# Performance work log

Measured on AMD Instinct MI355X. Metric: run time of the kernel, lower is better.

The kernel has to match this reference:

```python
import jax, jax.numpy as jnp
import numpy as np
from jax import lax

VOCAB = 27
N_EMBD = 512
D_MODEL = 256
PAD_IDX = 26
OUT = 1
B, T = 256, 512


def _lstm_layer(x, w_ih, w_hh, b_ih, b_hh):
    # x: [B, T, in]; w_ih: [4H, in]; w_hh: [4H, H]
    Bb = x.shape[0]
    H = w_hh.shape[1]
    # precompute input contribution to all gates for all timesteps
    xg = jnp.einsum('bti,gi->btg', x, w_ih) + b_ih + b_hh  # [B, T, 4H]

    def step(carry, xg_t):
        h, c = carry
        g = xg_t + h @ w_hh.T  # [B, 4H]
        i, f, gg, o = jnp.split(g, 4, axis=-1)  # PyTorch gate order i,f,g,o
        i = jax.nn.sigmoid(i)
        f = jax.nn.sigmoid(f)
        gg = jnp.tanh(gg)
        o = jax.nn.sigmoid(o)
        c = f * c + i * gg
        h = o * jnp.tanh(c)
        return (h, c), h

    h0 = jnp.zeros((Bb, H), dtype=x.dtype)
    c0 = jnp.zeros((Bb, H), dtype=x.dtype)
    _, ys = lax.scan(step, (h0, c0), jnp.swapaxes(xg, 0, 1))
    return jnp.swapaxes(ys, 0, 1)  # [B, T, H]


def setup_inputs() -> dict:
    key = jax.random.key(0)
    ks = jax.random.split(key, 16)
    s_e = 1.0  # nn.Embedding default init is N(0,1)
    emb = jax.random.normal(ks[0], (VOCAB, N_EMBD), dtype=jnp.float32)
    emb = emb.at[PAD_IDX].set(0.0)
    bound = 1.0 / np.sqrt(D_MODEL)

    def u(k, shape, b):
        return jax.random.uniform(k, shape, dtype=jnp.float32, minval=-b, maxval=b)

    inp = {
        'input_ids': jax.random.randint(ks[1], (B, T), 0, VOCAB, dtype=jnp.int64)
                      if jax.config.jax_enable_x64 else
                      jax.random.randint(ks[1], (B, T), 0, VOCAB).astype(jnp.int32),
        'emb': emb,
        'w_ih0': u(ks[2], (4 * D_MODEL, N_EMBD), bound),
        'w_hh0': u(ks[3], (4 * D_MODEL, D_MODEL), bound),
        'b_ih0': u(ks[4], (4 * D_MODEL,), bound),
        'b_hh0': u(ks[5], (4 * D_MODEL,), bound),
        'w_ih1': u(ks[6], (4 * D_MODEL, D_MODEL), bound),
        'w_hh1': u(ks[7], (4 * D_MODEL, D_MODEL), bound),
        'b_ih1': u(ks[8], (4 * D_MODEL,), bound),
        'b_hh1': u(ks[9], (4 * D_MODEL,), bound),
        'fc1_w': u(ks[10], (D_MODEL // 2, D_MODEL), bound),
        'fc1_b': u(ks[11], (D_MODEL // 2,), bound),
        'fc2_w': u(ks[12], (OUT, D_MODEL // 2), 1.0 / np.sqrt(D_MODEL // 2)),
        'fc2_b': u(ks[13], (OUT,), 1.0 / np.sqrt(D_MODEL // 2)),
    }
    return inp


def reference(input_ids, emb, w_ih0, w_hh0, b_ih0, b_hh0,
              w_ih1, w_hh1, b_ih1, b_hh1, fc1_w, fc1_b, fc2_w, fc2_b):
    # embedding with padding_idx: pad row forced to zero
    table = emb.at[PAD_IDX].set(0.0)
    x = table[input_ids]  # [B, T, n_embd]
    h1 = _lstm_layer(x, w_ih0, w_hh0, b_ih0, b_hh0)   # [B, T, H]
    h2 = _lstm_layer(h1, w_ih1, w_hh1, b_ih1, b_hh1)  # [B, T, H]
    last = h2[:, -1, :]                                # [B, H]
    hidden = jax.nn.relu(last @ fc1_w.T + fc1_b)
    logits = hidden @ fc2_w.T + fc2_b                  # [B, 1]
    return logits
```

## Files before the change

### kernel.cpp

```cpp
#include <hip/hip_runtime.h>

typedef unsigned short u16;
typedef unsigned int u32;
typedef unsigned long long u64;
typedef float f32x2 __attribute__((ext_vector_type(2)));

#define BATCH 256
#define TT 512
#define HID 256
#define GATES 1024
#define NEMB 512
#define VOC 27
#define HPAD 260

__device__ __forceinline__ float bf1(u16 x){ union{u32 u; float f;} v; v.u = ((u32)x) << 16; return v.f; }
__device__ __forceinline__ u16 f2bf(float f){
  union{float f; u32 u;} v; v.f = f;
  u32 u = v.u;
  return (u16)((u + 0x7fffu + ((u >> 16) & 1u)) >> 16);
}
__device__ __forceinline__ float sigm(float x){ return 1.f / (1.f + __expf(-x)); }
__device__ __forceinline__ f32x2 lo2(float4 v){ f32x2 r; r.x = v.x; r.y = v.y; return r; }
__device__ __forceinline__ f32x2 hi2(float4 v){ f32x2 r; r.x = v.z; r.y = v.w; return r; }

__global__ void k_detect(const u16* __restrict__ b, int* __restrict__ flag) {
  int bad = 0;
  for (int k = threadIdx.x; k < 512; k += 64)
    if (((b[2 * k] >> 7) & 0xFF) >= 127) bad = 1;
  unsigned long long m = __ballot(bad);
  if (threadIdx.x == 0) flag[0] = (m != 0ULL) ? 0 : 1;
}

__global__ void k_convert(const void* __restrict__ src, float* __restrict__ dst,
                          int n, const int* __restrict__ flag) {
  int i = blockIdx.x * 256 + threadIdx.x;
  if (i >= n) return;
  dst[i] = flag[0] ? bf1(((const u16*)src)[i]) : ((const float*)src)[i];
}

__global__ void k_prep(const void* __restrict__ emb, const void* __restrict__ wih,
                       const void* __restrict__ bih, const void* __restrict__ bhh,
                       const int* __restrict__ flag, float* __restrict__ W0) {
  int idx = blockIdx.x * 256 + threadIdx.x;
  if (idx >= VOC * GATES) return;
  int v = idx >> 10, g = idx & (GATES - 1);
  int isbf = flag[0];
  float acc = isbf ? (bf1(((const u16*)bih)[g]) + bf1(((const u16*)bhh)[g]))
                   : (((const float*)bih)[g] + ((const float*)bhh)[g]);
  if (v != 26) {
    float s = 0.f;
    if (isbf) {
      const u16* e = (const u16*)emb + v * NEMB;
      const u16* w = (const u16*)wih + g * NEMB;
      for (int i = 0; i < NEMB; i++) s = fmaf(bf1(e[i]), bf1(w[i]), s);
    } else {
      const float* e = (const float*)emb + v * NEMB;
      const float* w = (const float*)wih + g * NEMB;
      for (int i = 0; i < NEMB; i++) s = fmaf(e[i], w[i], s);
    }
    acc += s;
  }
  W0[idx] = acc;
}

__global__ __launch_bounds__(1024) void k_lstm(
    const int* __restrict__ ids, const float* __restrict__ W0,
    const float* __restrict__ whh0, const float* __restrict__ wih1,
    const float* __restrict__ whh1,
    const float* __restrict__ bih1, const float* __restrict__ bhh1,
    float* __restrict__ h0a, float* __restrict__ h0b,
    float* __restrict__ h1a, float* __restrict__ h1b,
    u32* __restrict__ bar)
{
  const int tid = threadIdx.x;
  const int bid = blockIdx.x;
  const int grp = ((bid >> 3) << 1) | (bid & 1);
  const int jq  = (bid & 7) >> 1;
  const int wv  = tid >> 6;
  const int ln  = tid & 63;

  const int tb = tid & 3;
  const int rr = tid >> 2;
  const int grow = (rr >> 6) * 256 + jq * 64 + (rr & 63);

  __shared__ __align__(16) float hp0[2][4][HPAD];
  __shared__ __align__(16) float hp1[4][HPAD];
  __shared__ float gs0[256][5];
  __shared__ float gs1[256][5];
  __shared__ int   ids_l[4][TT];

  const float* wl0 = whh0 + (size_t)grow * HID;
  const float* wi  = wih1 + (size_t)grow * HID;
  const float* wh  = whh1 + (size_t)grow * HID;
  const float bsum = bih1[grow] + bhh1[grow];

  const int pb = tid & 3, pj = (tid >> 2) & 63;
  const int prow = (grp * 4 + pb) * HID + (jq * 64 + pj);
  float c0r = 0.f, c1r = 0.f;

  u32* flags0 = bar;
  u32* flags1 = bar + 4096;

  #pragma unroll
  for (int u = 0; u < 2; ++u) {
    int e = tid + 1024 * u;
    int b = e >> 9, tt = e & 511;
    ids_l[b][tt] = ids[(grp * 4 + b) * TT + tt];
  }

  for (int t = 0; t <= TT + 1; ++t) {
    if (wv == 0) {
      const int q = ln & 3;
      const int pbid = ((bid >> 3) << 3) | (q << 1) | (bid & 1);
      u32 need = 0;
      const u32* fp = nullptr;
      if (ln < 4) {
        if (q != jq && t >= 1 && t <= TT) { fp = flags0 + pbid * 16; need = (u32)t; }
      } else if (ln < 8) {
        if (q != jq && t >= 3) { fp = flags1 + pbid * 16; need = (u32)(t - 2); }
      }
      for (;;) {
        bool ok = true;
        if (need) ok = __hip_atomic_load(fp, __ATOMIC_RELAXED, __HIP_MEMORY_SCOPE_AGENT) >= need;
        if (__all(ok)) break;
        __builtin_amdgcn_s_sleep(2);
      }
    }
    __syncthreads();

    if (tid < 512) {
      if (t <= TT) {
        const float* h0p = ((t + 1) & 1) ? h0b : h0a;
        const u64* s0 = (const u64*)h0p;
        int e = tid;
        u64 v = __hip_atomic_load(s0 + grp * 512 + e, __ATOMIC_RELAXED, __HIP_MEMORY_SCOPE_AGENT);
        *(u64*)&hp0[t & 1][e >> 7][(e & 127) * 2] = v;
      }
    } else {
      if (t >= 2) {
        const float* h1p = ((t + 1) & 1) ? h1b : h1a;
        const u64* s1 = (const u64*)h1p;
        int e = tid - 512;
        u64 v = __hip_atomic_load(s1 + grp * 512 + e, __ATOMIC_RELAXED, __HIP_MEMORY_SCOPE_AGENT);
        *(u64*)&hp1[e >> 7][(e & 127) * 2] = v;
      }
    }
    __syncthreads();

    if (t < TT) {
      float xgv = W0[(size_t)ids_l[tb][t] * GATES + grow];
      const float4* w4 = (const float4*)wl0;
      const float4* h4 = (const float4*)hp0[t & 1][tb];
      f32x2 sA = {0.f, 0.f}, sB = {0.f, 0.f};
      #pragma unroll 8
      for (int k = 0; k < 64; ++k) {
        float4 q = w4[k], hv = h4[k];
        sA = lo2(q) * lo2(hv) + sA;
        sB = hi2(q) * hi2(hv) + sB;
      }
      gs0[rr][tb] = xgv + sA.x + sA.y + sB.x + sB.y;
    }
    __syncthreads();

    if (t < TT && tid < 256) {
      float gi = sigm(gs0[pj][pb]);
      float gf = sigm(gs0[64 + pj][pb]);
      float gg = tanhf(gs0[128 + pj][pb]);
      float go = sigm(gs0[192 + pj][pb]);
      c0r = fmaf(gf, c0r, gi * gg);
      float* h0n = (t & 1) ? h0b : h0a;
      __hip_atomic_store(&h0n[prow], go * tanhf(c0r),
                         __ATOMIC_RELAXED, __HIP_MEMORY_SCOPE_AGENT);
    }
    __syncthreads();
    if (tid == 0 && t < TT)
      __hip_atomic_store(flags0 + bid * 16, (u32)(t + 1),
                         __ATOMIC_RELAXED, __HIP_MEMORY_SCOPE_AGENT);

    if (t >= 2) {
      const float4* wi4 = (const float4*)wi;
      const float4* wh4 = (const float4*)wh;
      const float4* x4  = (const float4*)hp0[(t - 1) & 1][tb];
      const float4* h4  = (const float4*)hp1[tb];
      f32x2 sIa = {0.f,0.f}, sIb = {0.f,0.f}, sHa = {0.f,0.f}, sHb = {0.f,0.f};
      #pragma unroll 8
      for (int k = 0; k < 64; ++k) {
        float4 qi = wi4[k], qh = wh4[k], xv = x4[k], hv = h4[k];
        sIa = lo2(qi) * lo2(xv) + sIa;
        sIb = hi2(qi) * hi2(xv) + sIb;
        sHa = lo2(qh) * lo2(hv) + sHa;
        sHb = hi2(qh) * hi2(hv) + sHb;
      }
      gs1[rr][tb] = bsum + sIa.x + sIa.y + sIb.x + sIb.y
                         + sHa.x + sHa.y + sHb.x + sHb.y;
    }
    __syncthreads();

    if (t >= 2 && tid < 256) {
      float gi = sigm(gs1[pj][pb]);
      float gf = sigm(gs1[64 + pj][pb]);
      float gg = tanhf(gs1[128 + pj][pb]);
      float go = sigm(gs1[192 + pj][pb]);
      c1r = fmaf(gf, c1r, gi * gg);
      float* h1n = (t & 1) ? h1b : h1a;
      __hip_atomic_store(&h1n[prow], go * tanhf(c1r),
                         __ATOMIC_RELAXED, __HIP_MEMORY_SCOPE_AGENT);
    }
    __syncthreads();
    if (tid == 0 && t >= 2 && t <= TT)
      __hip_atomic_store(flags1 + bid * 16, (u32)(t - 1),
                         __ATOMIC_RELAXED, __HIP_MEMORY_SCOPE_AGENT);
  }
}

__global__ __launch_bounds__(128) void k_fc(
    const float* __restrict__ hfin,
    const void* __restrict__ fc1w, const void* __restrict__ fc1b,
    const void* __restrict__ fc2w, const void* __restrict__ fc2b,
    const int* __restrict__ flag, void* __restrict__ out) {
  int b = blockIdx.x, j = threadIdx.x;
  __shared__ float red[128];
  const float* h = hfin + b * HID;
  int isbf = flag[0];
  float acc = isbf ? bf1(((const u16*)fc1b)[j]) : ((const float*)fc1b)[j];
  if (isbf) {
    const u16* w = (const u16*)fc1w + j * HID;
    for (int k = 0; k < HID; k++) acc = fmaf(bf1(w[k]), h[k], acc);
  } else {
    const float* w = (const float*)fc1w + j * HID;
    for (int k = 0; k < HID; k++) acc = fmaf(w[k], h[k], acc);
  }
  acc = fmaxf(acc, 0.f);
  float w2 = isbf ? bf1(((const u16*)fc2w)[j]) : ((const float*)fc2w)[j];
  red[j] = acc * w2;
  __syncthreads();
  for (int s = 64; s > 0; s >>= 1) {
    if (j < s) red[j] += red[j + s];
    __syncthreads();
  }
  if (j == 0) {
    float b2 = isbf ? bf1(((const u16*)fc2b)[0]) : ((const float*)fc2b)[0];
    float r = red[0] + b2;
    if (isbf) ((u16*)out)[b] = f2bf(r);
    else      ((float*)out)[b] = r;
  }
}

extern "C" void kernel_launch(void* const* d_in, const int* in_sizes, int n_in,
                              void* d_out, int out_size, void* d_ws, size_t ws_size,
                              hipStream_t stream) {
  const int* ids   = (const int*)d_in[0];
  const void* emb  = d_in[1];
  const void* wih0 = d_in[2];
  const void* whh0 = d_in[3];
  const void* bih0 = d_in[4];
  const void* bhh0 = d_in[5];
  const void* wih1 = d_in[6];
  const void* whh1 = d_in[7];
  const void* bih1 = d_in[8];
  const void* bhh1 = d_in[9];
  const void* fc1w = d_in[10];
  const void* fc1b = d_in[11];
  const void* fc2w = d_in[12];
  const void* fc2b = d_in[13];

  float* ws = (float*)d_ws;
  int*   flag    = (int*)ws;
  float* W0emb   = ws + 16;
  float* whh0_f  = W0emb  + VOC * GATES;
  float* wih1_f  = whh0_f + GATES * HID;
  float* whh1_f  = wih1_f + GATES * HID;
  float* bih1_f  = whh1_f + GATES * HID;
  float* bhh1_f  = bih1_f + GATES;
  float* h0A = bhh1_f + GATES;
  float* h0B = h0A + BATCH * HID;
  float* c0  = h0B + BATCH * HID;
  float* h1A = c0  + BATCH * HID;
  float* h1B = h1A + BATCH * HID;
  float* c1  = h1B + BATCH * HID;
  u32*   bar = (u32*)c0;

  k_detect<<<1, 64, 0, stream>>>((const u16*)bih0, flag);

  k_convert<<<(GATES * HID + 255) / 256, 256, 0, stream>>>(whh0, whh0_f, GATES * HID, flag);
  k_convert<<<(GATES * HID + 255) / 256, 256, 0, stream>>>(wih1, wih1_f, GATES * HID, flag);
  k_convert<<<(GATES * HID + 255) / 256, 256, 0, stream>>>(whh1, whh1_f, GATES * HID, flag);
  k_convert<<<(GATES + 255) / 256, 256, 0, stream>>>(bih1, bih1_f, GATES, flag);
  k_convert<<<(GATES + 255) / 256, 256, 0, stream>>>(bhh1, bhh1_f, GATES, flag);

  hipMemsetAsync(h0A, 0, (size_t)6 * BATCH * HID * sizeof(float), stream);

  k_prep<<<(VOC * GATES + 255) / 256, 256, 0, stream>>>(emb, wih0, bih0, bhh0, flag, W0emb);

  k_lstm<<<256, 1024, 0, stream>>>(ids, W0emb, whh0_f, wih1_f, whh1_f,
                                   bih1_f, bhh1_f, h0A, h0B, h1A, h1B, bar);

  k_fc<<<BATCH, 128, 0, stream>>>(h1B, fc1w, fc1b, fc2w, fc2b, flag, d_out);
}
```

Before: 12.44 ms.

## Split K across lanes with shuffle reduce and fuse gate nonlinearity per thread

Each thread now computes partial dot products for all four gates of one hidden unit over a quarter of K, then reduces across lanes with xor shuffles. The thread holding ks==0 applies the LSTM cell update directly. This removes the gs0/gs1 shared-memory staging and two __syncthreads per timestep, and the h buffers are padded per K-slice to avoid bank conflicts. The cost is four weight streams per thread, higher register pressure, and only a quarter of the threads doing the activation math.

```diff
diff --git a/kernel.cpp b/kernel.cpp
--- a/kernel.cpp
+++ b/kernel.cpp
@@ -11,7 +11,8 @@
 #define GATES 1024
 #define NEMB 512
 #define VOC 27
-#define HPAD 260
+#define KSF 68
+#define HROW 276
 
 __device__ __forceinline__ float bf1(u16 x){ union{u32 u; float f;} v; v.u = ((u32)x) << 16; return v.f; }
 __device__ __forceinline__ u16 f2bf(float f){
@@ -80,22 +81,35 @@
   const int ln  = tid & 63;
 
   const int tb = tid & 3;
-  const int rr = tid >> 2;
-  const int grow = (rr >> 6) * 256 + jq * 64 + (rr & 63);
-
-  __shared__ __align__(16) float hp0[2][4][HPAD];
-  __shared__ __align__(16) float hp1[4][HPAD];
-  __shared__ float gs0[256][5];
-  __shared__ float gs1[256][5];
+  const int ks = (tid >> 2) & 3;
+  const int j  = tid >> 4;
+
+  __shared__ __align__(16) float hp0[2][4][HROW];
+  __shared__ __align__(16) float hp1[4][HROW];
   __shared__ int   ids_l[4][TT];
 
-  const float* wl0 = whh0 + (size_t)grow * HID;
-  const float* wi  = wih1 + (size_t)grow * HID;
-  const float* wh  = whh1 + (size_t)grow * HID;
-  const float bsum = bih1[grow] + bhh1[grow];
-
-  const int pb = tid & 3, pj = (tid >> 2) & 63;
-  const int prow = (grp * 4 + pb) * HID + (jq * 64 + pj);
+  const int jj = jq * 64 + j;
+  const size_t r0 = (size_t)jj * HID + ks * 64;
+  const size_t rstep = (size_t)256 * HID;
+  const float4* wl0_0 = (const float4*)(whh0 + r0);
+  const float4* wl0_1 = (const float4*)(whh0 + r0 + rstep);
+  const float4* wl0_2 = (const float4*)(whh0 + r0 + 2 * rstep);
+  const float4* wl0_3 = (const float4*)(whh0 + r0 + 3 * rstep);
+  const float4* wi_0 = (const float4*)(wih1 + r0);
+  const float4* wi_1 = (const float4*)(wih1 + r0 + rstep);
+  const float4* wi_2 = (const float4*)(wih1 + r0 + 2 * rstep);
+  const float4* wi_3 = (const float4*)(wih1 + r0 + 3 * rstep);
+  const float4* wh_0 = (const float4*)(whh1 + r0);
+  const float4* wh_1 = (const float4*)(whh1 + r0 + rstep);
+  const float4* wh_2 = (const float4*)(whh1 + r0 + 2 * rstep);
+  const float4* wh_3 = (const float4*)(whh1 + r0 + 3 * rstep);
+
+  float bs[4];
+  #pragma unroll
+  for (int g = 0; g < 4; ++g) bs[g] = bih1[g * 256 + jj] + bhh1[g * 256 + jj];
+
+  const int prow = (grp * 4 + tb) * HID + jj;
+  const bool owner = (ks == 0);
   float c0r = 0.f, c1r = 0.f;
 
   u32* flags0 = bar;
@@ -133,44 +147,56 @@
         const float* h0p = ((t + 1) & 1) ? h0b : h0a;
         const u64* s0 = (const u64*)h0p;
         int e = tid;
+        int sb = e >> 7, f = (e & 127) * 2;
+        int mf = f + ((f >> 6) << 2);
         u64 v = __hip_atomic_load(s0 + grp * 512 + e, __ATOMIC_RELAXED, __HIP_MEMORY_SCOPE_AGENT);
-        *(u64*)&hp0[t & 1][e >> 7][(e & 127) * 2] = v;
+        *(u64*)&hp0[t & 1][sb][mf] = v;
       }
     } else {
       if (t >= 2) {
         const float* h1p = ((t + 1) & 1) ? h1b : h1a;
         const u64* s1 = (const u64*)h1p;
         int e = tid - 512;
+        int sb = e >> 7, f = (e & 127) * 2;
+        int mf = f + ((f >> 6) << 2);
         u64 v = __hip_atomic_load(s1 + grp * 512 + e, __ATOMIC_RELAXED, __HIP_MEMORY_SCOPE_AGENT);
-        *(u64*)&hp1[e >> 7][(e & 127) * 2] = v;
+        *(u64*)&hp1[sb][mf] = v;
       }
     }
     __syncthreads();
 
     if (t < TT) {
-      float xgv = W0[(size_t)ids_l[tb][t] * GATES + grow];
-      const float4* w4 = (const float4*)wl0;
-      const float4* h4 = (const float4*)hp0[t & 1][tb];
-      f32x2 sA = {0.f, 0.f}, sB = {0.f, 0.f};
-      #pragma unroll 8
-      for (int k = 0; k < 64; ++k) {
-        float4 q = w4[k], hv = h4[k];
-        sA = lo2(q) * lo2(hv) + sA;
-        sB = hi2(q) * hi2(hv) + sB;
-      }
-      gs0[rr][tb] = xgv + sA.x + sA.y + sB.x + sB.y;
-    }
-    __syncthreads();
-
-    if (t < TT && tid < 256) {
-      float gi = sigm(gs0[pj][pb]);
-      float gf = sigm(gs0[64 + pj][pb]);
-      float gg = tanhf(gs0[128 + pj][pb]);
-      float go = sigm(gs0[192 + pj][pb]);
-      c0r = fmaf(gf, c0r, gi * gg);
-      float* h0n = (t & 1) ? h0b : h0a;
-      __hip_atomic_store(&h0n[prow], go * tanhf(c0r),
-                         __ATOMIC_RELAXED, __HIP_MEMORY_SCOPE_AGENT);
+      const float4* h4 = (const float4*)&hp0[t & 1][tb][ks * KSF];
+      f32x2 aL0={0,0}, aH0={0,0}, aL1={0,0}, aH1={0,0};
+      f32x2 aL2={0,0}, aH2={0,0}, aL3={0,0}, aH3={0,0};
+      #pragma unroll 4
+      for (int k = 0; k < 16; ++k) {
+        float4 hv = h4[k];
+        float4 q0 = wl0_0[k], q1 = wl0_1[k], q2 = wl0_2[k], q3 = wl0_3[k];
+        aL0 = lo2(q0) * lo2(hv) + aL0; aH0 = hi2(q0) * hi2(hv) + aH0;
+        aL1 = lo2(q1) * lo2(hv) + aL1; aH1 = hi2(q1) * hi2(hv) + aH1;
+        aL2 = lo2(q2) * lo2(hv) + aL2; aH2 = hi2(q2) * hi2(hv) + aH2;
+        aL3 = lo2(q3) * lo2(hv) + aL3; aH3 = hi2(q3) * hi2(hv) + aH3;
+      }
+      float s0 = aL0.x + aL0.y + aH0.x + aH0.y;
+      float s1 = aL1.x + aL1.y + aH1.x + aH1.y;
+      float s2 = aL2.x + aL2.y + aH2.x + aH2.y;
+      float s3 = aL3.x + aL3.y + aH3.x + aH3.y;
+      s0 += __shfl_xor(s0, 4); s0 += __shfl_xor(s0, 8);
+      s1 += __shfl_xor(s1, 4); s1 += __shfl_xor(s1, 8);
+      s2 += __shfl_xor(s2, 4); s2 += __shfl_xor(s2, 8);
+      s3 += __shfl_xor(s3, 4); s3 += __shfl_xor(s3, 8);
+      if (owner) {
+        const float* xr = W0 + (size_t)ids_l[tb][t] * GATES + jj;
+        float gi = sigm(s0 + xr[0]);
+        float gf = sigm(s1 + xr[256]);
+        float gg = tanhf(s2 + xr[512]);
+        float go = sigm(s3 + xr[768]);
+        c0r = fmaf(gf, c0r, gi * gg);
+        float* h0n = (t & 1) ? h0b : h0a;
+        __hip_atomic_store(&h0n[prow], go * tanhf(c0r),
+                           __ATOMIC_RELAXED, __HIP_MEMORY_SCOPE_AGENT);
+      }
     }
     __syncthreads();
     if (tid == 0 && t < TT)
@@ -178,33 +204,42 @@
                          __ATOMIC_RELAXED, __HIP_MEMORY_SCOPE_AGENT);
 
     if (t >= 2) {
-      const float4* wi4 = (const float4*)wi;
-      const float4* wh4 = (const float4*)wh;
-      const float4* x4  = (const float4*)hp0[(t - 1) & 1][tb];
-      const float4* h4  = (const float4*)hp1[tb];
-      f32x2 sIa = {0.f,0.f}, sIb = {0.f,0.f}, sHa = {0.f,0.f}, sHb = {0.f,0.f};
-      #pragma unroll 8
-      for (int k = 0; k < 64; ++k) {
-        float4 qi = wi4[k], qh = wh4[k], xv = x4[k], hv = h4[k];
-        sIa = lo2(qi) * lo2(xv) + sIa;
-        sIb = hi2(qi) * hi2(xv) + sIb;
-        sHa = lo2(qh) * lo2(hv) + sHa;
-        sHb = hi2(qh) * hi2(hv) + sHb;
-      }
-      gs1[rr][tb] = bsum + sIa.x + sIa.y + sIb.x + sIb.y
-                         + sHa.x + sHa.y + sHb.x + sHb.y;
-    }
-    __syncthreads();
-
-    if (t >= 2 && tid < 256) {
-      float gi = sigm(gs1[pj][pb]);
-      float gf = sigm(gs1[64 + pj][pb]);
-      float gg = tanhf(gs1[128 + pj][pb]);
-      float go = sigm(gs1[192 + pj][pb]);
-      c1r = fmaf(gf, c1r, gi * gg);
-      float* h1n = (t & 1) ? h1b : h1a;
-      __hip_atomic_store(&h1n[prow], go * tanhf(c1r),
-                         __ATOMIC_RELAXED, __HIP_MEMORY_SCOPE_AGENT);
+      const float4* x4 = (const float4*)&hp0[(t - 1) & 1][tb][ks * KSF];
+      const float4* h4 = (const float4*)&hp1[tb][ks * KSF];
+      f32x2 aL0={0,0}, aH0={0,0}, aL1={0,0}, aH1={0,0};
+      f32x2 aL2={0,0}, aH2={0,0}, aL3={0,0}, aH3={0,0};
+      #pragma unroll 2
+      for (int k = 0; k < 16; ++k) {
+        float4 xv = x4[k], hv = h4[k];
+        float4 qi0 = wi_0[k], qi1 = wi_1[k], qi2 = wi_2[k], qi3 = wi_3[k];
+        aL0 = lo2(qi0) * lo2(xv) + aL0; aH0 = hi2(qi0) * hi2(xv) + aH0;
+        aL1 = lo2(qi1) * lo2(xv) + aL1; aH1 = hi2(qi1) * hi2(xv) + aH1;
+        aL2 = lo2(qi2) * lo2(xv) + aL2; aH2 = hi2(qi2) * hi2(xv) + aH2;
+        aL3 = lo2(qi3) * lo2(xv) + aL3; aH3 = hi2(qi3) * hi2(xv) + aH3;
+        float4 qh0 = wh_0[k], qh1 = wh_1[k], qh2 = wh_2[k], qh3 = wh_3[k];
+        aL0 = lo2(qh0) * lo2(hv) + aL0; aH0 = hi2(qh0) * hi2(hv) + aH0;
+        aL1 = lo2(qh1) * lo2(hv) + aL1; aH1 = hi2(qh1) * hi2(hv) + aH1;
+        aL2 = lo2(qh2) * lo2(hv) + aL2; aH2 = hi2(qh2) * hi2(hv) + aH2;
+        aL3 = lo2(qh3) * lo2(hv) + aL3; aH3 = hi2(qh3) * hi2(hv) + aH3;
+      }
+      float s0 = aL0.x + aL0.y + aH0.x + aH0.y;
+      float s1 = aL1.x + aL1.y + aH1.x + aH1.y;
+      float s2 = aL2.x + aL2.y + aH2.x + aH2.y;
+      float s3 = aL3.x + aL3.y + aH3.x + aH3.y;
+      s0 += __shfl_xor(s0, 4); s0 += __shfl_xor(s0, 8);
+      s1 += __shfl_xor(s1, 4); s1 += __shfl_xor(s1, 8);
+      s2 += __shfl_xor(s2, 4); s2 += __shfl_xor(s2, 8);
+      s3 += __shfl_xor(s3, 4); s3 += __shfl_xor(s3, 8);
+      if (owner) {
+        float gi = sigm(s0 + bs[0]);
+        float gf = sigm(s1 + bs[1]);
+        float gg = tanhf(s2 + bs[2]);
+        float go = sigm(s3 + bs[3]);
+        c1r = fmaf(gf, c1r, gi * gg);
+        float* h1n = (t & 1) ? h1b : h1a;
+        __hip_atomic_store(&h1n[prow], go * tanhf(c1r),
+                           __ATOMIC_RELAXED, __HIP_MEMORY_SCOPE_AGENT);
+      }
     }
     __syncthreads();
     if (tid == 0 && t >= 2 && t <= TT)
```

Result: slower. 18.59 ms (+49.4%).

## Split block into concurrent layer-0 and layer-1 halves, two gate rows per thread

Applied to the files above, without the earlier changes.

Threads 0-511 now compute the layer-0 recurrent gate matvec while threads 512-1023 compute the layer-1 gate matvec in the same phase, each thread handling two gate rows that share one h vector load. This removes a separate compute phase and one __syncthreads per timestep, and reuses each LDS h load across two weight rows. In exchange the per-thread work doubles and the two halves are unbalanced (layer 1 does twice the FLOPs), so the critical path per step may lengthen and register pressure rises.

```diff
diff --git a/kernel.cpp b/kernel.cpp
--- a/kernel.cpp
+++ b/kernel.cpp
@@ -80,8 +80,7 @@
   const int ln  = tid & 63;
 
   const int tb = tid & 3;
-  const int rr = tid >> 2;
-  const int grow = (rr >> 6) * 256 + jq * 64 + (rr & 63);
+  const int pr = (tid >> 2) & 127;
 
   __shared__ __align__(16) float hp0[2][4][HPAD];
   __shared__ __align__(16) float hp1[4][HPAD];
@@ -89,10 +88,17 @@
   __shared__ float gs1[256][5];
   __shared__ int   ids_l[4][TT];
 
-  const float* wl0 = whh0 + (size_t)grow * HID;
-  const float* wi  = wih1 + (size_t)grow * HID;
-  const float* wh  = whh1 + (size_t)grow * HID;
-  const float bsum = bih1[grow] + bhh1[grow];
+  const int grow0 = ((pr >> 6) << 8) + jq * 64 + (pr & 63);
+  const int grow1 = grow0 + 512;
+
+  const float4* wl0a = (const float4*)(whh0 + (size_t)grow0 * HID);
+  const float4* wl0b = (const float4*)(whh0 + (size_t)grow1 * HID);
+  const float4* wiA = (const float4*)(wih1 + (size_t)grow0 * HID);
+  const float4* wiB = (const float4*)(wih1 + (size_t)grow1 * HID);
+  const float4* whA = (const float4*)(whh1 + (size_t)grow0 * HID);
+  const float4* whB = (const float4*)(whh1 + (size_t)grow1 * HID);
+  const float bsA = bih1[grow0] + bhh1[grow0];
+  const float bsB = bih1[grow1] + bhh1[grow1];
 
   const int pb = tid & 3, pj = (tid >> 2) & 63;
   const int prow = (grp * 4 + pb) * HID + (jq * 64 + pj);
@@ -147,18 +153,41 @@
     }
     __syncthreads();
 
-    if (t < TT) {
-      float xgv = W0[(size_t)ids_l[tb][t] * GATES + grow];
-      const float4* w4 = (const float4*)wl0;
-      const float4* h4 = (const float4*)hp0[t & 1][tb];
-      f32x2 sA = {0.f, 0.f}, sB = {0.f, 0.f};
-      #pragma unroll 8
-      for (int k = 0; k < 64; ++k) {
-        float4 q = w4[k], hv = h4[k];
-        sA = lo2(q) * lo2(hv) + sA;
-        sB = hi2(q) * hi2(hv) + sB;
-      }
-      gs0[rr][tb] = xgv + sA.x + sA.y + sB.x + sB.y;
+    if (tid < 512) {
+      if (t < TT) {
+        const float* xr = W0 + (size_t)ids_l[tb][t] * GATES;
+        float xg0 = xr[grow0], xg1 = xr[grow1];
+        const float4* h4 = (const float4*)hp0[t & 1][tb];
+        f32x2 aL0={0,0}, aH0={0,0}, aL1={0,0}, aH1={0,0};
+        #pragma unroll 8
+        for (int k = 0; k < 64; ++k) {
+          float4 hv = h4[k];
+          float4 q0 = wl0a[k], q1 = wl0b[k];
+          aL0 = lo2(q0) * lo2(hv) + aL0; aH0 = hi2(q0) * hi2(hv) + aH0;
+          aL1 = lo2(q1) * lo2(hv) + aL1; aH1 = hi2(q1) * hi2(hv) + aH1;
+        }
+        gs0[pr][tb]       = xg0 + aL0.x + aL0.y + aH0.x + aH0.y;
+        gs0[pr + 128][tb] = xg1 + aL1.x + aL1.y + aH1.x + aH1.y;
+      }
+    } else {
+      if (t >= 2) {
+        const float4* x4 = (const float4*)hp0[(t - 1) & 1][tb];
+        const float4* h4 = (const float4*)hp1[tb];
+        f32x2 aL0={0,0}, aH0={0,0}, aL1={0,0}, aH1={0,0};
+        #pragma unroll 8
+        for (int k = 0; k < 64; ++k) {
+          float4 xv = x4[k];
+          float4 qi0 = wiA[k], qi1 = wiB[k];
+          aL0 = lo2(qi0) * lo2(xv) + aL0; aH0 = hi2(qi0) * hi2(xv) + aH0;
+          aL1 = lo2(qi1) * lo2(xv) + aL1; aH1 = hi2(qi1) * hi2(xv) + aH1;
+          float4 hv = h4[k];
+          float4 qh0 = whA[k], qh1 = whB[k];
+          aL0 = lo2(qh0) * lo2(hv) + aL0; aH0 = hi2(qh0) * hi2(hv) + aH0;
+          aL1 = lo2(qh1) * lo2(hv) + aL1; aH1 = hi2(qh1) * hi2(hv) + aH1;
+        }
+        gs1[pr][tb]       = bsA + aL0.x + aL0.y + aH0.x + aH0.y;
+        gs1[pr + 128][tb] = bsB + aL1.x + aL1.y + aH1.x + aH1.y;
+      }
     }
     __syncthreads();
 
@@ -176,25 +205,6 @@
     if (tid == 0 && t < TT)
       __hip_atomic_store(flags0 + bid * 16, (u32)(t + 1),
                          __ATOMIC_RELAXED, __HIP_MEMORY_SCOPE_AGENT);
-
-    if (t >= 2) {
-      const float4* wi4 = (const float4*)wi;
-      const float4* wh4 = (const float4*)wh;
-      const float4* x4  = (const float4*)hp0[(t - 1) & 1][tb];
-      const float4* h4  = (const float4*)hp1[tb];
-      f32x2 sIa = {0.f,0.f}, sIb = {0.f,0.f}, sHa = {0.f,0.f}, sHb = {0.f,0.f};
-      #pragma unroll 8
-      for (int k = 0; k < 64; ++k) {
-        float4 qi = wi4[k], qh = wh4[k], xv = x4[k], hv = h4[k];
-        sIa = lo2(qi) * lo2(xv) + sIa;
-        sIb = hi2(qi) * hi2(xv) + sIb;
-        sHa = lo2(qh) * lo2(hv) + sHa;
-        sHb = hi2(qh) * hi2(hv) + sHb;
-      }
-      gs1[rr][tb] = bsum + sIa.x + sIa.y + sIb.x + sIb.y
-                         + sHa.x + sHa.y + sHb.x + sHb.y;
-    }
-    __syncthreads();
 
     if (t >= 2 && tid < 256) {
       float gi = sigm(gs1[pj][pb]);
```

Result: slower. 13.17 ms (+5.9%).
